# Performance work log

Hardware: AMD Instinct MI355X
Metric: run time of the kernel (lower is better)

The kernel has to match this reference:

```python
import jax, jax.numpy as jnp
import numpy as np

EMBED_DIM = 128
NUM_CLASSES = 2
NUM_NODES = 100000
NUM_EDGES = 500000


def setup_inputs() -> dict:
    key = jax.random.key(0)
    k1, k2, k3, k4, k5, k6 = jax.random.split(key, 6)
    node_embed = jax.random.normal(k1, (NUM_NODES, EMBED_DIM), dtype=jnp.float32)
    edge_index = jax.random.randint(k2, (2, NUM_EDGES), 0, NUM_NODES, dtype=jnp.int64)
    # MLP params (torch Linear default init scale ~ 1/sqrt(fan_in))
    s1 = 1.0 / np.sqrt(2 * EMBED_DIM)
    s2 = 1.0 / np.sqrt(EMBED_DIM)
    W1 = jax.random.uniform(k3, (2 * EMBED_DIM, EMBED_DIM), jnp.float32, -s1, s1)
    b1 = jax.random.uniform(k4, (EMBED_DIM,), jnp.float32, -s1, s1)
    W2 = jax.random.uniform(k5, (EMBED_DIM, NUM_CLASSES), jnp.float32, -s2, s2)
    b2 = jax.random.uniform(k6, (NUM_CLASSES,), jnp.float32, -s2, s2)
    return {"node_embed": node_embed, "edge_index": edge_index,
            "W1": W1, "b1": b1, "W2": W2, "b2": b2}


def reference(node_embed, edge_index, W1, b1, W2, b2):
    row, col = edge_index[0], edge_index[1]
    # Gather endpoint embeddings and concat -> [num_edges, 2*embed_dim]
    edge_feat = jnp.concatenate([node_embed[row], node_embed[col]], axis=1)
    h = jax.nn.relu(edge_feat @ W1 + b1)  # [num_edges, embed_dim]
    # Dropout(0.1) is identity in eval mode.
    return h @ W2 + b2  # [num_edges, num_classes]
```

## Files before the change

### kernel.cpp

```cpp
#include <hip/hip_runtime.h>
#include <hip/hip_bf16.h>


#define EMBED 128

typedef _Float16 half8 __attribute__((ext_vector_type(8)));
typedef _Float16 half4 __attribute__((ext_vector_type(4)));
typedef float floatx4 __attribute__((ext_vector_type(4)));

__global__ __launch_bounds__(256) void prep(
    const float* __restrict__ W1, const float* __restrict__ W2,
    const float* __restrict__ b1, const int* __restrict__ idx,
    _Float16* __restrict__ WT, _Float16* __restrict__ W2PT,
    _Float16* __restrict__ b1f, int* __restrict__ flag) {
    if (blockIdx.x < 128) {
        __shared__ float lds[16][17];
        const int ty = threadIdx.x >> 4, tx = threadIdx.x & 15;
        const int r0 = (blockIdx.x >> 3) * 16;
        const int c0 = (blockIdx.x & 7) * 16;
        lds[ty][tx] = W1[(r0 + ty) * 128 + c0 + tx];
        __syncthreads();
        const int jbase = c0 + (r0 >= 128 ? 128 : 0);
        const int kbase = r0 & 127;
        WT[(size_t)(jbase + ty) * 128 + kbase + tx] = (_Float16)lds[tx][ty];
    } else {
        const int t = threadIdx.x;
        if (t < 64) {
            const int hw = idx[2 * t + 1];
            const unsigned long long m = __ballot(hw != 0);
            if (t == 0) *flag = (m == 0ull) ? 1 : 0;
        }
        if (t < 128) b1f[t] = (_Float16)b1[t];
        for (int i = t; i < 2048; i += 256) {
            const int n = i >> 7, k = i & 127;
            W2PT[i] = (n < 2) ? (_Float16)W2[k * 2 + n] : (_Float16)0.f;
        }
    }
}

__global__ __launch_bounds__(256) void gemm_ab(
    const float* __restrict__ X, const _Float16* __restrict__ WT,
    _Float16* __restrict__ AB, int n_nodes, int n_tiles) {
    __shared__ _Float16 sh[64 * 264];
    _Float16* xs   = sh;
    _Float16* outs = sh;
    const int t = threadIdx.x;
    const int w = t >> 6, lane = t & 63, lm = lane & 15, quad = lane >> 4;

    int srow[8], scol[8];
#pragma unroll
    for (int i = 0; i < 8; ++i) {
        const int flat = i * 1024 + t * 4;
        srow[i] = flat >> 7;
        scol[i] = flat & 127;
    }

    int T = blockIdx.x;
    float4 pf[8];
    if (T < n_tiles) {
#pragma unroll
        for (int i = 0; i < 8; ++i) {
            int node = T * 64 + srow[i];
            if (node > n_nodes - 1) node = n_nodes - 1;
            pf[i] = *(const float4*)(X + (size_t)node * EMBED + scol[i]);
        }
    }

    for (; T < n_tiles; T += gridDim.x) {
        const int mblk = T * 64;

#pragma unroll
        for (int i = 0; i < 8; ++i) {
            half4 h;
            h[0] = (_Float16)pf[i].x; h[1] = (_Float16)pf[i].y;
            h[2] = (_Float16)pf[i].z; h[3] = (_Float16)pf[i].w;
            *(half4*)(xs + srow[i] * 136 + scol[i]) = h;
        }
        __syncthreads();

        const int Tn = T + gridDim.x;
        if (Tn < n_tiles) {
#pragma unroll
            for (int i = 0; i < 8; ++i) {
                int node = Tn * 64 + srow[i];
                if (node > n_nodes - 1) node = n_nodes - 1;
                pf[i] = *(const float4*)(X + (size_t)node * EMBED + scol[i]);
            }
        }

        floatx4 acc[4][4];
#pragma unroll
        for (int a = 0; a < 4; ++a)
#pragma unroll
            for (int b = 0; b < 4; ++b)
                acc[a][b] = (floatx4){0.f, 0.f, 0.f, 0.f};

#pragma unroll
        for (int ks = 0; ks < 4; ++ks) {
            const int k0 = ks * 32 + quad * 8;
            half8 xf[4];
#pragma unroll
            for (int mf = 0; mf < 4; ++mf)
                xf[mf] = *(const half8*)(xs + (mf * 16 + lm) * 136 + k0);
#pragma unroll
            for (int jf = 0; jf < 4; ++jf) {
                const int j = w * 64 + jf * 16 + lm;
                const half8 wf = *(const half8*)(WT + (size_t)j * EMBED + k0);
#pragma unroll
                for (int mf = 0; mf < 4; ++mf)
                    acc[mf][jf] = __builtin_amdgcn_mfma_f32_16x16x32_f16(wf, xf[mf], acc[mf][jf], 0, 0, 0);
            }
        }
        __syncthreads();

#pragma unroll
        for (int mf = 0; mf < 4; ++mf) {
#pragma unroll
            for (int jf = 0; jf < 4; ++jf) {
                half4 h;
#pragma unroll
                for (int r = 0; r < 4; ++r) h[r] = (_Float16)acc[mf][jf][r];
                *(half4*)(outs + (mf * 16 + lm) * 264 + w * 64 + jf * 16 + quad * 4) = h;
            }
        }
        __syncthreads();

#pragma unroll
        for (int i = 0; i < 8; ++i) {
            const int idx8 = i * 256 + t;
            const int node = idx8 >> 5, jj = idx8 & 31;
            if (mblk + node < n_nodes)
                *(half8*)(AB + (size_t)(mblk + node) * 256 + jj * 8) =
                    *(const half8*)(outs + node * 264 + jj * 8);
        }
        __syncthreads();
    }
}

__global__ __launch_bounds__(256) void edge_mlp(
    const _Float16* __restrict__ AB, const int* __restrict__ eidx,
    const int* __restrict__ flag, const _Float16* __restrict__ b1f,
    const _Float16* __restrict__ W2PT, const float* __restrict__ b2,
    float* __restrict__ out, int n_edges) {
    const int lane = threadIdx.x & 63, lm = lane & 15, quad = lane >> 4;
    const int ebase = (blockIdx.x * 4 + (threadIdx.x >> 6)) * 32;
    if (ebase >= n_edges) return;

    const int mode = *flag;
    int e0 = ebase + lm, e1 = ebase + 16 + lm;
    if (e0 > n_edges - 1) e0 = n_edges - 1;
    if (e1 > n_edges - 1) e1 = n_edges - 1;
    int row0, col0, row1, col1;
    if (mode) {
        row0 = eidx[2 * (size_t)e0];
        col0 = eidx[2 * ((size_t)n_edges + e0)];
        row1 = eidx[2 * (size_t)e1];
        col1 = eidx[2 * ((size_t)n_edges + e1)];
    } else {
        row0 = eidx[e0];
        col0 = eidx[(size_t)n_edges + e0];
        row1 = eidx[e1];
        col1 = eidx[(size_t)n_edges + e1];
    }

    const _Float16* a0p = AB + (size_t)row0 * 256;
    const _Float16* b0p = AB + (size_t)col0 * 256 + 128;
    const _Float16* a1p = AB + (size_t)row1 * 256;
    const _Float16* b1p = AB + (size_t)col1 * 256 + 128;

    half8 a0[4], b0[4], a1[4], b1[4];
#pragma unroll
    for (int ks = 0; ks < 4; ++ks) {
        const int k0 = ks * 32 + quad * 8;
        a0[ks] = *(const half8*)(a0p + k0);
        b0[ks] = *(const half8*)(b0p + k0);
        a1[ks] = *(const half8*)(a1p + k0);
        b1[ks] = *(const half8*)(b1p + k0);
    }

    floatx4 acc0 = (floatx4){0.f, 0.f, 0.f, 0.f};
    floatx4 acc1 = (floatx4){0.f, 0.f, 0.f, 0.f};
#pragma unroll
    for (int ks = 0; ks < 4; ++ks) {
        const int k0 = ks * 32 + quad * 8;
        const half8 bi = *(const half8*)(b1f + k0);
        const half8 wv = *(const half8*)(W2PT + lm * 128 + k0);
        half8 h0 = a0[ks] + b0[ks] + bi;
        half8 h1 = a1[ks] + b1[ks] + bi;
#pragma unroll
        for (int j = 0; j < 8; ++j) {
            h0[j] = h0[j] > (_Float16)0.f ? h0[j] : (_Float16)0.f;
            h1[j] = h1[j] > (_Float16)0.f ? h1[j] : (_Float16)0.f;
        }
        acc0 = __builtin_amdgcn_mfma_f32_16x16x32_f16(h0, wv, acc0, 0, 0, 0);
        acc1 = __builtin_amdgcn_mfma_f32_16x16x32_f16(h1, wv, acc1, 0, 0, 0);
    }

    if (lm < 2) {
        const float b2v = b2[lm];
#pragma unroll
        for (int r = 0; r < 4; ++r) {
            const int ed0 = ebase + quad * 4 + r;
            const int ed1 = ebase + 16 + quad * 4 + r;
            if (ed0 < n_edges) out[(size_t)ed0 * 2 + lm] = acc0[r] + b2v;
            if (ed1 < n_edges) out[(size_t)ed1 * 2 + lm] = acc1[r] + b2v;
        }
    }
}

extern "C" void kernel_launch(void* const* d_in, const int* in_sizes, int n_in,
                              void* d_out, int out_size, void* d_ws, size_t ws_size,
                              hipStream_t stream) {
    const float* X   = (const float*)d_in[0];
    const int*   idx = (const int*)d_in[1];
    const float* W1  = (const float*)d_in[2];
    const float* b1  = (const float*)d_in[3];
    const float* W2  = (const float*)d_in[4];
    const float* b2  = (const float*)d_in[5];
    float* out = (float*)d_out;

    const int n_nodes = in_sizes[0] / EMBED;
    const int n_edges = in_sizes[1] / 2;

    char* ws = (char*)d_ws;
    int*      flag = (int*)ws;
    _Float16* AB   = (_Float16*)(ws + 256);
    _Float16* WT   = (_Float16*)(ws + 256 + (size_t)n_nodes * 512);
    _Float16* W2PT = WT + 256 * 128;
    _Float16* b1f  = W2PT + 16 * 128;

    const int n_tiles = (n_nodes + 63) / 64;

    prep<<<129, 256, 0, stream>>>(W1, W2, b1, idx, WT, W2PT, b1f, flag);
    gemm_ab<<<782, 256, 0, stream>>>(X, WT, AB, n_nodes, n_tiles);
    edge_mlp<<<(n_edges + 127) / 128, 256, 0, stream>>>(
        AB, idx, flag, b1f, W2PT, b2, out, n_edges);
}
```

Measured before the change: 154.2 us.

## Make edge MLP persistent with index prefetch and nontemporal loads/stores

Rewrites edge_mlp as a grid-stride persistent kernel on 1280 blocks. Each wave prefetches the next group's edge indices while the current group's gathers and MFMAs run, and keeps the W2 fragments in registers across iterations. It also switches the streaming index loads, output stores and the node-embedding loads in gemm_ab to nontemporal accesses to reduce cache pollution. In exchange there are fewer waves in flight for hiding gather latency, and the launch-bounds occupancy hint may constrain registers.

```diff
diff --git a/kernel.cpp b/kernel.cpp
--- a/kernel.cpp
+++ b/kernel.cpp
@@ -56,13 +56,14 @@
     }
 
     int T = blockIdx.x;
-    float4 pf[8];
+    floatx4 pf[8];
     if (T < n_tiles) {
 #pragma unroll
         for (int i = 0; i < 8; ++i) {
             int node = T * 64 + srow[i];
             if (node > n_nodes - 1) node = n_nodes - 1;
-            pf[i] = *(const float4*)(X + (size_t)node * EMBED + scol[i]);
+            pf[i] = __builtin_nontemporal_load(
+                (const floatx4*)(X + (size_t)node * EMBED + scol[i]));
         }
     }
 
@@ -72,8 +73,8 @@
 #pragma unroll
         for (int i = 0; i < 8; ++i) {
             half4 h;
-            h[0] = (_Float16)pf[i].x; h[1] = (_Float16)pf[i].y;
-            h[2] = (_Float16)pf[i].z; h[3] = (_Float16)pf[i].w;
+            h[0] = (_Float16)pf[i][0]; h[1] = (_Float16)pf[i][1];
+            h[2] = (_Float16)pf[i][2]; h[3] = (_Float16)pf[i][3];
             *(half4*)(xs + srow[i] * 136 + scol[i]) = h;
         }
         __syncthreads();
@@ -84,7 +85,8 @@
             for (int i = 0; i < 8; ++i) {
                 int node = Tn * 64 + srow[i];
                 if (node > n_nodes - 1) node = n_nodes - 1;
-                pf[i] = *(const float4*)(X + (size_t)node * EMBED + scol[i]);
+                pf[i] = __builtin_nontemporal_load(
+                    (const floatx4*)(X + (size_t)node * EMBED + scol[i]));
             }
         }
 
@@ -137,74 +139,97 @@
     }
 }
 
-__global__ __launch_bounds__(256) void edge_mlp(
+__global__ __launch_bounds__(256, 4) void edge_mlp(
     const _Float16* __restrict__ AB, const int* __restrict__ eidx,
     const int* __restrict__ flag, const _Float16* __restrict__ b1f,
     const _Float16* __restrict__ W2PT, const float* __restrict__ b2,
     float* __restrict__ out, int n_edges) {
     const int lane = threadIdx.x & 63, lm = lane & 15, quad = lane >> 4;
-    const int ebase = (blockIdx.x * 4 + (threadIdx.x >> 6)) * 32;
-    if (ebase >= n_edges) return;
+    const int W = gridDim.x * 4;
+    const int G = (n_edges + 31) / 32;
+    int g = blockIdx.x * 4 + (threadIdx.x >> 6);
+    if (g >= G) return;
 
     const int mode = *flag;
-    int e0 = ebase + lm, e1 = ebase + 16 + lm;
-    if (e0 > n_edges - 1) e0 = n_edges - 1;
-    if (e1 > n_edges - 1) e1 = n_edges - 1;
+    const float b2v = b2[lm & 1];
+
+    half8 wv[4];
+#pragma unroll
+    for (int ks = 0; ks < 4; ++ks)
+        wv[ks] = *(const half8*)(W2PT + lm * 128 + ks * 32 + quad * 8);
+
+    auto load_idx = [&](int gg, int& r0, int& c0, int& r1, int& c1) {
+        int e0 = gg * 32 + lm, e1 = gg * 32 + 16 + lm;
+        if (e0 > n_edges - 1) e0 = n_edges - 1;
+        if (e1 > n_edges - 1) e1 = n_edges - 1;
+        if (mode) {
+            r0 = __builtin_nontemporal_load(eidx + 2 * (size_t)e0);
+            c0 = __builtin_nontemporal_load(eidx + 2 * ((size_t)n_edges + e0));
+            r1 = __builtin_nontemporal_load(eidx + 2 * (size_t)e1);
+            c1 = __builtin_nontemporal_load(eidx + 2 * ((size_t)n_edges + e1));
+        } else {
+            r0 = __builtin_nontemporal_load(eidx + e0);
+            c0 = __builtin_nontemporal_load(eidx + (size_t)n_edges + e0);
+            r1 = __builtin_nontemporal_load(eidx + e1);
+            c1 = __builtin_nontemporal_load(eidx + (size_t)n_edges + e1);
+        }
+    };
+
     int row0, col0, row1, col1;
-    if (mode) {
-        row0 = eidx[2 * (size_t)e0];
-        col0 = eidx[2 * ((size_t)n_edges + e0)];
-        row1 = eidx[2 * (size_t)e1];
-        col1 = eidx[2 * ((size_t)n_edges + e1)];
-    } else {
-        row0 = eidx[e0];
-        col0 = eidx[(size_t)n_edges + e0];
-        row1 = eidx[e1];
-        col1 = eidx[(size_t)n_edges + e1];
-    }
-
-    const _Float16* a0p = AB + (size_t)row0 * 256;
-    const _Float16* b0p = AB + (size_t)col0 * 256 + 128;
-    const _Float16* a1p = AB + (size_t)row1 * 256;
-    const _Float16* b1p = AB + (size_t)col1 * 256 + 128;
-
-    half8 a0[4], b0[4], a1[4], b1[4];
-#pragma unroll
-    for (int ks = 0; ks < 4; ++ks) {
-        const int k0 = ks * 32 + quad * 8;
-        a0[ks] = *(const half8*)(a0p + k0);
-        b0[ks] = *(const half8*)(b0p + k0);
-        a1[ks] = *(const half8*)(a1p + k0);
-        b1[ks] = *(const half8*)(b1p + k0);
-    }
-
-    floatx4 acc0 = (floatx4){0.f, 0.f, 0.f, 0.f};
-    floatx4 acc1 = (floatx4){0.f, 0.f, 0.f, 0.f};
-#pragma unroll
-    for (int ks = 0; ks < 4; ++ks) {
-        const int k0 = ks * 32 + quad * 8;
-        const half8 bi = *(const half8*)(b1f + k0);
-        const half8 wv = *(const half8*)(W2PT + lm * 128 + k0);
-        half8 h0 = a0[ks] + b0[ks] + bi;
-        half8 h1 = a1[ks] + b1[ks] + bi;
-#pragma unroll
-        for (int j = 0; j < 8; ++j) {
-            h0[j] = h0[j] > (_Float16)0.f ? h0[j] : (_Float16)0.f;
-            h1[j] = h1[j] > (_Float16)0.f ? h1[j] : (_Float16)0.f;
-        }
-        acc0 = __builtin_amdgcn_mfma_f32_16x16x32_f16(h0, wv, acc0, 0, 0, 0);
-        acc1 = __builtin_amdgcn_mfma_f32_16x16x32_f16(h1, wv, acc1, 0, 0, 0);
-    }
-
-    if (lm < 2) {
-        const float b2v = b2[lm];
-#pragma unroll
-        for (int r = 0; r < 4; ++r) {
-            const int ed0 = ebase + quad * 4 + r;
-            const int ed1 = ebase + 16 + quad * 4 + r;
-            if (ed0 < n_edges) out[(size_t)ed0 * 2 + lm] = acc0[r] + b2v;
-            if (ed1 < n_edges) out[(size_t)ed1 * 2 + lm] = acc1[r] + b2v;
-        }
+    load_idx(g, row0, col0, row1, col1);
+
+    for (;;) {
+        const _Float16* a0p = AB + (size_t)row0 * 256;
+        const _Float16* b0p = AB + (size_t)col0 * 256 + 128;
+        const _Float16* a1p = AB + (size_t)row1 * 256;
+        const _Float16* c1p = AB + (size_t)col1 * 256 + 128;
+        half8 a0[4], b0[4], a1[4], c1[4];
+#pragma unroll
+        for (int ks = 0; ks < 4; ++ks) {
+            const int k0 = ks * 32 + quad * 8;
+            a0[ks] = *(const half8*)(a0p + k0);
+            b0[ks] = *(const half8*)(b0p + k0);
+            a1[ks] = *(const half8*)(a1p + k0);
+            c1[ks] = *(const half8*)(c1p + k0);
+        }
+
+        const int gn = g + W;
+        int nr0 = 0, nc0 = 0, nr1 = 0, nc1 = 0;
+        if (gn < G) load_idx(gn, nr0, nc0, nr1, nc1);
+
+        floatx4 acc0 = (floatx4){0.f, 0.f, 0.f, 0.f};
+        floatx4 acc1 = (floatx4){0.f, 0.f, 0.f, 0.f};
+#pragma unroll
+        for (int ks = 0; ks < 4; ++ks) {
+            const int k0 = ks * 32 + quad * 8;
+            const half8 bi = *(const half8*)(b1f + k0);
+            half8 h0 = a0[ks] + b0[ks] + bi;
+            half8 h1 = a1[ks] + c1[ks] + bi;
+#pragma unroll
+            for (int j = 0; j < 8; ++j) {
+                h0[j] = h0[j] > (_Float16)0.f ? h0[j] : (_Float16)0.f;
+                h1[j] = h1[j] > (_Float16)0.f ? h1[j] : (_Float16)0.f;
+            }
+            acc0 = __builtin_amdgcn_mfma_f32_16x16x32_f16(h0, wv[ks], acc0, 0, 0, 0);
+            acc1 = __builtin_amdgcn_mfma_f32_16x16x32_f16(h1, wv[ks], acc1, 0, 0, 0);
+        }
+
+        if (lm < 2) {
+            const int ebase = g * 32;
+#pragma unroll
+            for (int r = 0; r < 4; ++r) {
+                const int ed0 = ebase + quad * 4 + r;
+                const int ed1 = ebase + 16 + quad * 4 + r;
+                if (ed0 < n_edges)
+                    __builtin_nontemporal_store(acc0[r] + b2v, out + (size_t)ed0 * 2 + lm);
+                if (ed1 < n_edges)
+                    __builtin_nontemporal_store(acc1[r] + b2v, out + (size_t)ed1 * 2 + lm);
+            }
+        }
+
+        if (gn >= G) break;
+        g = gn;
+        row0 = nr0; col0 = nc0; row1 = nr1; col1 = nc1;
     }
 }
 
@@ -233,6 +258,6 @@
 
     prep<<<129, 256, 0, stream>>>(W1, W2, b1, idx, WT, W2PT, b1f, flag);
     gemm_ab<<<782, 256, 0, stream>>>(X, WT, AB, n_nodes, n_tiles);
-    edge_mlp<<<(n_edges + 127) / 128, 256, 0, stream>>>(
+    edge_mlp<<<1280, 256, 0, stream>>>(
         AB, idx, flag, b1f, W2PT, b2, out, n_edges);
 }
```

Result: slower. 160.8 us (+4.3%).

## Make edge_mlp persistent with software-pipelined index and gather prefetch

Applied to the files above, without the earlier changes.

The edge MLP kernel becomes a grid-stride persistent kernel with 768 blocks. Each wave now handles 16 edges per step and double-buffers its work: it loads the edge indices two groups ahead and gathers the next group's AB rows while computing the current group's MFMA. W2 and b1 fragments are loaded once per wave instead of once per step. This aims to hide the latency of the random gathers and cut launch and tail overhead, at the cost of fewer edges in flight per wave and more registers under the launch_bounds(256,3) occupancy target.

```diff
diff --git a/kernel.cpp b/kernel.cpp
--- a/kernel.cpp
+++ b/kernel.cpp
@@ -137,74 +137,99 @@
     }
 }
 
-__global__ __launch_bounds__(256) void edge_mlp(
+__global__ __launch_bounds__(256, 3) void edge_mlp(
     const _Float16* __restrict__ AB, const int* __restrict__ eidx,
     const int* __restrict__ flag, const _Float16* __restrict__ b1f,
     const _Float16* __restrict__ W2PT, const float* __restrict__ b2,
     float* __restrict__ out, int n_edges) {
     const int lane = threadIdx.x & 63, lm = lane & 15, quad = lane >> 4;
-    const int ebase = (blockIdx.x * 4 + (threadIdx.x >> 6)) * 32;
-    if (ebase >= n_edges) return;
+    const int W = gridDim.x * 4;
+    const int G = (n_edges + 15) / 16;
+    const int wid = blockIdx.x * 4 + (threadIdx.x >> 6);
+    if (wid >= G) return;
 
     const int mode = *flag;
-    int e0 = ebase + lm, e1 = ebase + 16 + lm;
-    if (e0 > n_edges - 1) e0 = n_edges - 1;
-    if (e1 > n_edges - 1) e1 = n_edges - 1;
-    int row0, col0, row1, col1;
-    if (mode) {
-        row0 = eidx[2 * (size_t)e0];
-        col0 = eidx[2 * ((size_t)n_edges + e0)];
-        row1 = eidx[2 * (size_t)e1];
-        col1 = eidx[2 * ((size_t)n_edges + e1)];
-    } else {
-        row0 = eidx[e0];
-        col0 = eidx[(size_t)n_edges + e0];
-        row1 = eidx[e1];
-        col1 = eidx[(size_t)n_edges + e1];
-    }
-
-    const _Float16* a0p = AB + (size_t)row0 * 256;
-    const _Float16* b0p = AB + (size_t)col0 * 256 + 128;
-    const _Float16* a1p = AB + (size_t)row1 * 256;
-    const _Float16* b1p = AB + (size_t)col1 * 256 + 128;
-
-    half8 a0[4], b0[4], a1[4], b1[4];
+    const float b2v = b2[lm & 1];
+
+    half8 wv[4], bv[4];
 #pragma unroll
     for (int ks = 0; ks < 4; ++ks) {
-        const int k0 = ks * 32 + quad * 8;
-        a0[ks] = *(const half8*)(a0p + k0);
-        b0[ks] = *(const half8*)(b0p + k0);
-        a1[ks] = *(const half8*)(a1p + k0);
-        b1[ks] = *(const half8*)(b1p + k0);
-    }
-
-    floatx4 acc0 = (floatx4){0.f, 0.f, 0.f, 0.f};
-    floatx4 acc1 = (floatx4){0.f, 0.f, 0.f, 0.f};
-#pragma unroll
-    for (int ks = 0; ks < 4; ++ks) {
-        const int k0 = ks * 32 + quad * 8;
-        const half8 bi = *(const half8*)(b1f + k0);
-        const half8 wv = *(const half8*)(W2PT + lm * 128 + k0);
-        half8 h0 = a0[ks] + b0[ks] + bi;
-        half8 h1 = a1[ks] + b1[ks] + bi;
-#pragma unroll
-        for (int j = 0; j < 8; ++j) {
-            h0[j] = h0[j] > (_Float16)0.f ? h0[j] : (_Float16)0.f;
-            h1[j] = h1[j] > (_Float16)0.f ? h1[j] : (_Float16)0.f;
-        }
-        acc0 = __builtin_amdgcn_mfma_f32_16x16x32_f16(h0, wv, acc0, 0, 0, 0);
-        acc1 = __builtin_amdgcn_mfma_f32_16x16x32_f16(h1, wv, acc1, 0, 0, 0);
-    }
-
-    if (lm < 2) {
-        const float b2v = b2[lm];
-#pragma unroll
-        for (int r = 0; r < 4; ++r) {
-            const int ed0 = ebase + quad * 4 + r;
-            const int ed1 = ebase + 16 + quad * 4 + r;
-            if (ed0 < n_edges) out[(size_t)ed0 * 2 + lm] = acc0[r] + b2v;
-            if (ed1 < n_edges) out[(size_t)ed1 * 2 + lm] = acc1[r] + b2v;
-        }
+        wv[ks] = *(const half8*)(W2PT + lm * 128 + ks * 32 + quad * 8);
+        bv[ks] = *(const half8*)(b1f + ks * 32 + quad * 8);
+    }
+
+    auto ldidx = [&](int g, int& r, int& c) {
+        int e = g * 16 + lm;
+        if (e > n_edges - 1) e = n_edges - 1;
+        if (mode) {
+            r = eidx[2 * (size_t)e];
+            c = eidx[2 * ((size_t)n_edges + e)];
+        } else {
+            r = eidx[e];
+            c = eidx[(size_t)n_edges + e];
+        }
+    };
+
+    auto gather = [&](int r, int c, half8* d) {
+        const _Float16* ap = AB + (size_t)r * 256;
+        const _Float16* bp = AB + (size_t)c * 256 + 128;
+#pragma unroll
+        for (int ks = 0; ks < 4; ++ks) {
+            const int k0 = ks * 32 + quad * 8;
+            d[ks]     = *(const half8*)(ap + k0);
+            d[ks + 4] = *(const half8*)(bp + k0);
+        }
+    };
+
+    auto comp = [&](int g, const half8* d) {
+        floatx4 acc = (floatx4){0.f, 0.f, 0.f, 0.f};
+#pragma unroll
+        for (int ks = 0; ks < 4; ++ks) {
+            half8 h = d[ks] + d[ks + 4] + bv[ks];
+#pragma unroll
+            for (int j = 0; j < 8; ++j)
+                h[j] = h[j] > (_Float16)0.f ? h[j] : (_Float16)0.f;
+            acc = __builtin_amdgcn_mfma_f32_16x16x32_f16(h, wv[ks], acc, 0, 0, 0);
+        }
+        if (lm < 2) {
+            const int eb = g * 16;
+#pragma unroll
+            for (int r = 0; r < 4; ++r) {
+                const int ed = eb + quad * 4 + r;
+                if (ed < n_edges) out[(size_t)ed * 2 + lm] = acc[r] + b2v;
+            }
+        }
+    };
+
+    int g0 = wid;
+    int g1 = g0 + W;
+    bool h1 = g1 < G;
+    int r0, c0, r1, c1;
+    ldidx(g0, r0, c0);
+    if (h1) ldidx(g1, r1, c1);
+    half8 a0[8], a1[8];
+    gather(r0, c0, a0);
+
+    for (;;) {
+        const int g2 = g1 + W;
+        const bool h2 = h1 && (g2 < G);
+        if (h1) {
+            if (h2) ldidx(g2, r0, c0);
+            gather(r1, c1, a1);
+        }
+        comp(g0, a0);
+        if (!h1) break;
+
+        const int g3 = g2 + W;
+        const bool h3 = h2 && (g3 < G);
+        if (h2) {
+            if (h3) ldidx(g3, r1, c1);
+            gather(r0, c0, a0);
+        }
+        comp(g1, a1);
+        if (!h2) break;
+
+        g0 = g2; g1 = g3; h1 = h3;
     }
 }
 
@@ -233,6 +258,6 @@
 
     prep<<<129, 256, 0, stream>>>(W1, W2, b1, idx, WT, W2PT, b1f, flag);
     gemm_ab<<<782, 256, 0, stream>>>(X, WT, AB, n_nodes, n_tiles);
-    edge_mlp<<<(n_edges + 127) / 128, 256, 0, stream>>>(
+    edge_mlp<<<768, 256, 0, stream>>>(
         AB, idx, flag, b1f, W2PT, b2, out, n_edges);
 }
```

Measured after the change: 147.1 us. 4.6% less time.

## Sort edges by source node via counting sort before edge MLP gather

Applied to the files above, without the earlier changes.

Adds a histogram, two-level scan and atomic scatter that bucket edges by row index, so the edge MLP reads row embeddings with better cache locality. The edge kernel is restructured so each wave processes 16 groups of 16 edges in a loop, prefetching the next indices, and writes outputs back through the original edge permutation. This adds four extra kernel launches plus atomic traffic over 500k edges, and the final output stores become scattered instead of contiguous.

```diff
diff --git a/kernel.cpp b/kernel.cpp
--- a/kernel.cpp
+++ b/kernel.cpp
@@ -7,12 +7,14 @@
 typedef _Float16 half8 __attribute__((ext_vector_type(8)));
 typedef _Float16 half4 __attribute__((ext_vector_type(4)));
 typedef float floatx4 __attribute__((ext_vector_type(4)));
+typedef int intx4 __attribute__((ext_vector_type(4)));
 
 __global__ __launch_bounds__(256) void prep(
     const float* __restrict__ W1, const float* __restrict__ W2,
     const float* __restrict__ b1, const int* __restrict__ idx,
     _Float16* __restrict__ WT, _Float16* __restrict__ W2PT,
-    _Float16* __restrict__ b1f, int* __restrict__ flag) {
+    _Float16* __restrict__ b1f, int* __restrict__ flag,
+    int* __restrict__ cnt) {
     if (blockIdx.x < 128) {
         __shared__ float lds[16][17];
         const int ty = threadIdx.x >> 4, tx = threadIdx.x & 15;
@@ -23,7 +25,7 @@
         const int jbase = c0 + (r0 >= 128 ? 128 : 0);
         const int kbase = r0 & 127;
         WT[(size_t)(jbase + ty) * 128 + kbase + tx] = (_Float16)lds[tx][ty];
-    } else {
+    } else if (blockIdx.x == 128) {
         const int t = threadIdx.x;
         if (t < 64) {
             const int hw = idx[2 * t + 1];
@@ -35,6 +37,86 @@
             const int n = i >> 7, k = i & 127;
             W2PT[i] = (n < 2) ? (_Float16)W2[k * 2 + n] : (_Float16)0.f;
         }
+    } else {
+        const int i = (blockIdx.x - 129) * 256 + threadIdx.x;
+        ((intx4*)cnt)[i] = (intx4){0, 0, 0, 0};
+    }
+}
+
+__global__ __launch_bounds__(256) void hist(
+    const int* __restrict__ eidx, const int* __restrict__ flag,
+    int* __restrict__ cnt, int n_edges) {
+    const int mode = *flag;
+    for (int e = blockIdx.x * 256 + threadIdx.x; e < n_edges;
+         e += gridDim.x * 256) {
+        const int r = eidx[(size_t)e << mode];
+        atomicAdd(&cnt[r], 1);
+    }
+}
+
+__global__ __launch_bounds__(1024) void scan1(
+    int* __restrict__ cnt, int* __restrict__ bsum, int nn) {
+    __shared__ int wsums[16];
+    const int t = threadIdx.x, lane = t & 63, w = t >> 6;
+    const int i = blockIdx.x * 1024 + t;
+    const int v = (i < nn) ? cnt[i] : 0;
+    int x = v;
+#pragma unroll
+    for (int d = 1; d < 64; d <<= 1) {
+        const int y = __shfl_up(x, d, 64);
+        if (lane >= d) x += y;
+    }
+    if (lane == 63) wsums[w] = x;
+    __syncthreads();
+    if (w == 0 && lane < 16) {
+        const int s = wsums[lane];
+        int xs = s;
+#pragma unroll
+        for (int d = 1; d < 16; d <<= 1) {
+            const int y = __shfl_up(xs, d, 64);
+            if (lane >= d) xs += y;
+        }
+        wsums[lane] = xs - s;
+    }
+    __syncthreads();
+    if (i < nn) cnt[i] = x - v + wsums[w];
+    if (t == 1023) bsum[blockIdx.x] = x + wsums[15];
+}
+
+__global__ __launch_bounds__(128) void scan2(
+    int* __restrict__ bsum, int nb, int* __restrict__ sR,
+    int* __restrict__ sC, int* __restrict__ sE, int n_edges, int g16) {
+    __shared__ int wtot[2];
+    const int t = threadIdx.x, lane = t & 63, w = t >> 6;
+    const int v = (t < nb) ? bsum[t] : 0;
+    int x = v;
+#pragma unroll
+    for (int d = 1; d < 64; d <<= 1) {
+        const int y = __shfl_up(x, d, 64);
+        if (lane >= d) x += y;
+    }
+    if (lane == 63) wtot[w] = x;
+    __syncthreads();
+    const int excl = x - v + (w == 1 ? wtot[0] : 0);
+    if (t < nb) bsum[t] = excl;
+    if (t < 16) {
+        const int p = n_edges + t;
+        if (p < g16) { sR[p] = 0; sC[p] = 0; sE[p] = 0; }
+    }
+}
+
+__global__ __launch_bounds__(256) void scatter(
+    const int* __restrict__ eidx, const int* __restrict__ flag,
+    int* __restrict__ pos, const int* __restrict__ boff,
+    int* __restrict__ sR, int* __restrict__ sC, int* __restrict__ sE,
+    int n_edges) {
+    const int mode = *flag;
+    for (int e = blockIdx.x * 256 + threadIdx.x; e < n_edges;
+         e += gridDim.x * 256) {
+        const int r = eidx[(size_t)e << mode];
+        const int c = eidx[((size_t)n_edges + e) << mode];
+        const int p = atomicAdd(&pos[r], 1) + boff[r >> 10];
+        sR[p] = r; sC[p] = c; sE[p] = e;
     }
 }
 
@@ -137,73 +219,77 @@
     }
 }
 
-__global__ __launch_bounds__(256) void edge_mlp(
-    const _Float16* __restrict__ AB, const int* __restrict__ eidx,
-    const int* __restrict__ flag, const _Float16* __restrict__ b1f,
-    const _Float16* __restrict__ W2PT, const float* __restrict__ b2,
-    float* __restrict__ out, int n_edges) {
+#define NPW 16
+__global__ __launch_bounds__(256, 3) void edge_mlp(
+    const _Float16* __restrict__ AB, const int* __restrict__ sR,
+    const int* __restrict__ sC, const int* __restrict__ sE,
+    const _Float16* __restrict__ b1f, const _Float16* __restrict__ W2PT,
+    const float* __restrict__ b2, float* __restrict__ out, int n_edges) {
     const int lane = threadIdx.x & 63, lm = lane & 15, quad = lane >> 4;
-    const int ebase = (blockIdx.x * 4 + (threadIdx.x >> 6)) * 32;
-    if (ebase >= n_edges) return;
-
-    const int mode = *flag;
-    int e0 = ebase + lm, e1 = ebase + 16 + lm;
-    if (e0 > n_edges - 1) e0 = n_edges - 1;
-    if (e1 > n_edges - 1) e1 = n_edges - 1;
-    int row0, col0, row1, col1;
-    if (mode) {
-        row0 = eidx[2 * (size_t)e0];
-        col0 = eidx[2 * ((size_t)n_edges + e0)];
-        row1 = eidx[2 * (size_t)e1];
-        col1 = eidx[2 * ((size_t)n_edges + e1)];
-    } else {
-        row0 = eidx[e0];
-        col0 = eidx[(size_t)n_edges + e0];
-        row1 = eidx[e1];
-        col1 = eidx[(size_t)n_edges + e1];
-    }
-
-    const _Float16* a0p = AB + (size_t)row0 * 256;
-    const _Float16* b0p = AB + (size_t)col0 * 256 + 128;
-    const _Float16* a1p = AB + (size_t)row1 * 256;
-    const _Float16* b1p = AB + (size_t)col1 * 256 + 128;
-
-    half8 a0[4], b0[4], a1[4], b1[4];
+    const int G = (n_edges + 15) / 16;
+    const int wid = blockIdx.x * 4 + (threadIdx.x >> 6);
+    const int base = wid * NPW;
+    if (base >= G) return;
+
+    const float b2v = b2[lm & 1];
+
+    half8 wv[4], bvv[4];
 #pragma unroll
     for (int ks = 0; ks < 4; ++ks) {
-        const int k0 = ks * 32 + quad * 8;
-        a0[ks] = *(const half8*)(a0p + k0);
-        b0[ks] = *(const half8*)(b0p + k0);
-        a1[ks] = *(const half8*)(a1p + k0);
-        b1[ks] = *(const half8*)(b1p + k0);
-    }
-
-    floatx4 acc0 = (floatx4){0.f, 0.f, 0.f, 0.f};
-    floatx4 acc1 = (floatx4){0.f, 0.f, 0.f, 0.f};
-#pragma unroll
-    for (int ks = 0; ks < 4; ++ks) {
-        const int k0 = ks * 32 + quad * 8;
-        const half8 bi = *(const half8*)(b1f + k0);
-        const half8 wv = *(const half8*)(W2PT + lm * 128 + k0);
-        half8 h0 = a0[ks] + b0[ks] + bi;
-        half8 h1 = a1[ks] + b1[ks] + bi;
-#pragma unroll
-        for (int j = 0; j < 8; ++j) {
-            h0[j] = h0[j] > (_Float16)0.f ? h0[j] : (_Float16)0.f;
-            h1[j] = h1[j] > (_Float16)0.f ? h1[j] : (_Float16)0.f;
-        }
-        acc0 = __builtin_amdgcn_mfma_f32_16x16x32_f16(h0, wv, acc0, 0, 0, 0);
-        acc1 = __builtin_amdgcn_mfma_f32_16x16x32_f16(h1, wv, acc1, 0, 0, 0);
-    }
-
-    if (lm < 2) {
-        const float b2v = b2[lm];
-#pragma unroll
-        for (int r = 0; r < 4; ++r) {
-            const int ed0 = ebase + quad * 4 + r;
-            const int ed1 = ebase + 16 + quad * 4 + r;
-            if (ed0 < n_edges) out[(size_t)ed0 * 2 + lm] = acc0[r] + b2v;
-            if (ed1 < n_edges) out[(size_t)ed1 * 2 + lm] = acc1[r] + b2v;
+        wv[ks]  = *(const half8*)(W2PT + lm * 128 + ks * 32 + quad * 8);
+        bvv[ks] = *(const half8*)(b1f + ks * 32 + quad * 8);
+    }
+
+    auto cg = [&](int g) { return g < G ? g : G - 1; };
+
+    int r0 = sR[cg(base) * 16 + lm],     c0 = sC[cg(base) * 16 + lm];
+    int r1 = sR[cg(base + 1) * 16 + lm], c1 = sC[cg(base + 1) * 16 + lm];
+
+    for (int k = 0; k < NPW; k += 2) {
+        const int g0 = cg(base + k), g1 = cg(base + k + 1);
+
+        const _Float16* a0p = AB + (size_t)(unsigned)r0 * 256 + quad * 8;
+        const _Float16* b0p = AB + (size_t)(unsigned)c0 * 256 + 128 + quad * 8;
+        const _Float16* a1p = AB + (size_t)(unsigned)r1 * 256 + quad * 8;
+        const _Float16* b1p = AB + (size_t)(unsigned)c1 * 256 + 128 + quad * 8;
+        half8 d0[8], d1[8];
+#pragma unroll
+        for (int ks = 0; ks < 4; ++ks) {
+            d0[ks]     = *(const half8*)(a0p + ks * 32);
+            d0[ks + 4] = *(const half8*)(b0p + ks * 32);
+            d1[ks]     = *(const half8*)(a1p + ks * 32);
+            d1[ks + 4] = *(const half8*)(b1p + ks * 32);
+        }
+        const intx4 e0 = *(const intx4*)(sE + g0 * 16 + quad * 4);
+        const intx4 e1 = *(const intx4*)(sE + g1 * 16 + quad * 4);
+
+        const int gn0 = cg(base + k + 2), gn1 = cg(base + k + 3);
+        r0 = sR[gn0 * 16 + lm]; c0 = sC[gn0 * 16 + lm];
+        r1 = sR[gn1 * 16 + lm]; c1 = sC[gn1 * 16 + lm];
+
+        floatx4 acc0 = (floatx4){0.f, 0.f, 0.f, 0.f};
+        floatx4 acc1 = (floatx4){0.f, 0.f, 0.f, 0.f};
+#pragma unroll
+        for (int ks = 0; ks < 4; ++ks) {
+            half8 h0 = d0[ks] + d0[ks + 4] + bvv[ks];
+            half8 h1 = d1[ks] + d1[ks + 4] + bvv[ks];
+#pragma unroll
+            for (int j = 0; j < 8; ++j) {
+                h0[j] = h0[j] > (_Float16)0.f ? h0[j] : (_Float16)0.f;
+                h1[j] = h1[j] > (_Float16)0.f ? h1[j] : (_Float16)0.f;
+            }
+            acc0 = __builtin_amdgcn_mfma_f32_16x16x32_f16(h0, wv[ks], acc0, 0, 0, 0);
+            acc1 = __builtin_amdgcn_mfma_f32_16x16x32_f16(h1, wv[ks], acc1, 0, 0, 0);
+        }
+
+        if (lm < 2) {
+#pragma unroll
+            for (int r = 0; r < 4; ++r) {
+                const int i0 = r == 0 ? e0[0] : r == 1 ? e0[1] : r == 2 ? e0[2] : e0[3];
+                const int i1 = r == 0 ? e1[0] : r == 1 ? e1[1] : r == 2 ? e1[2] : e1[3];
+                out[(size_t)(unsigned)i0 * 2 + lm] = acc0[r] + b2v;
+                out[(size_t)(unsigned)i1 * 2 + lm] = acc1[r] + b2v;
+            }
         }
     }
 }
@@ -222,17 +308,33 @@
     const int n_nodes = in_sizes[0] / EMBED;
     const int n_edges = in_sizes[1] / 2;
 
+    const int NB  = (n_nodes + 1023) / 1024;
+    const int G   = (n_edges + 15) / 16;
+    const int G16 = G * 16;
+
     char* ws = (char*)d_ws;
     int*      flag = (int*)ws;
     _Float16* AB   = (_Float16*)(ws + 256);
     _Float16* WT   = (_Float16*)(ws + 256 + (size_t)n_nodes * 512);
     _Float16* W2PT = WT + 256 * 128;
     _Float16* b1f  = W2PT + 16 * 128;
+    char* p = (char*)(b1f + 128);
+    p = (char*)(((uintptr_t)p + 255) & ~(uintptr_t)255);
+    int*   cnt  = (int*)p;              p += (size_t)NB * 1024 * 4;
+    int*   bsum = (int*)p;              p += 1024;
+    int*   sR   = (int*)p;              p += (size_t)G16 * 4;
+    int*   sC   = (int*)p;              p += (size_t)G16 * 4;
+    int*   sE   = (int*)p;              p += (size_t)G16 * 4;
 
     const int n_tiles = (n_nodes + 63) / 64;
 
-    prep<<<129, 256, 0, stream>>>(W1, W2, b1, idx, WT, W2PT, b1f, flag);
+    prep<<<129 + NB, 256, 0, stream>>>(W1, W2, b1, idx, WT, W2PT, b1f, flag, cnt);
     gemm_ab<<<782, 256, 0, stream>>>(X, WT, AB, n_nodes, n_tiles);
-    edge_mlp<<<(n_edges + 127) / 128, 256, 0, stream>>>(
-        AB, idx, flag, b1f, W2PT, b2, out, n_edges);
-}
+    hist<<<256, 256, 0, stream>>>(idx, flag, cnt, n_edges);
+    scan1<<<NB, 1024, 0, stream>>>(cnt, bsum, n_nodes);
+    scan2<<<1, 128, 0, stream>>>(bsum, NB, sR, sC, sE, n_edges, G16);
+    scatter<<<256, 256, 0, stream>>>(idx, flag, cnt, bsum, sR, sC, sE, n_edges);
+    const int nblk = (G + 4 * NPW - 1) / (4 * NPW);
+    edge_mlp<<<nblk, 256, 0, stream>>>(
+        AB, sR, sC, sE, b1f, W2PT, b2, out, n_edges);
+}
```

Measured after the change: 194.1 us. 1.26x slower.
